# Optimization experiments

Hardware: AMD Instinct MI355X
Metric: run time of the kernel (lower is better)

Reference implementation:

```python
import jax, jax.numpy as jnp
import numpy as np

NF4 = jnp.array([-1.0, -0.6961928009986877, -0.5250730514526367, -0.39491748809814453,
                 -0.28444138169288635, -0.18477343022823334, -0.09105003625154495, 0.0,
                 0.07958029955625534, 0.16093020141124725, 0.24611230194568634,
                 0.33791524171829224, 0.44070982933044434, 0.5626170039176941,
                 0.7229568362236023, 1.0], dtype=jnp.float32)
BLOCK_SIZE = 64
SCALING = 32.0 / 16.0  # alpha / rank


def setup_inputs() -> dict:
    key = jax.random.key(0)
    k = jax.random.split(key, 6)
    B, S, IN, OUT, R = 4, 128, 4096, 11008, 16
    n_blocks = (OUT * IN) // BLOCK_SIZE  # 704512, exact (no padding needed)
    return {
        "x": jax.random.normal(k[0], (B, S, IN), jnp.float32),
        "weight_indices": jax.random.randint(k[1], (OUT, IN), 0, 16, dtype=jnp.int32),
        "weight_scales": jax.random.uniform(k[2], (n_blocks,), jnp.float32),
        "lora_A": jax.random.normal(k[3], (IN, R), jnp.float32),
        "lora_B": jax.random.normal(k[4], (R, OUT), jnp.float32),
        "bias": jax.random.normal(k[5], (OUT,), jnp.float32),
    }


def dequantize_nf4(indices, scales, shape):
    # LUT gather then blockwise absmax scale
    w = NF4[indices.reshape(-1)]                    # [out*in]
    w = w.reshape(-1, BLOCK_SIZE) * scales[:, None]  # [n_blocks, block]
    return w.reshape(shape)                          # [out, in]


def reference(x, weight_indices, weight_scales, lora_A, lora_B, bias):
    W = dequantize_nf4(weight_indices, weight_scales, weight_indices.shape)  # [out, in]
    base = jnp.einsum("bsi,oi->bso", x, W) + bias                            # F.linear
    lora = (x @ lora_A) @ lora_B                                             # low-rank path (dropout p=0 -> identity)
    return base + lora * SCALING
```

## Files before the change

kernel.cpp:

```cpp
#include <hip/hip_runtime.h>
#include <stdint.h>

typedef __bf16 bf16x8 __attribute__((ext_vector_type(8)));
typedef float f32x4 __attribute__((ext_vector_type(4)));
typedef unsigned short ushort_t;

#define N_OUT 11008
#define K_DIM 4096
#define M_DIM 512
#define BM 256
#define BN 64
#define BK 64
#define KHALF 2048
#define NT 32

__constant__ float c_nf4[16] = {
    -1.0f, -0.6961928009986877f, -0.5250730514526367f, -0.39491748809814453f,
    -0.28444138169288635f, -0.18477343022823334f, -0.09105003625154495f, 0.0f,
    0.07958029955625534f, 0.16093020141124725f, 0.24611230194568634f,
    0.33791524171829224f, 0.44070982933044434f, 0.5626170039176941f,
    0.7229568362236023f, 1.0f};

__device__ __forceinline__ uint32_t pkbf(float lo, float hi) {
  uint32_t ul = __builtin_bit_cast(uint32_t, lo);
  uint32_t uh = __builtin_bit_cast(uint32_t, hi);
  return ((ul + 0x8000u) >> 16) | ((uh + 0x8000u) & 0xffff0000u);
}

__device__ __forceinline__ void async16(const void* g, void* l) {
  __builtin_amdgcn_global_load_lds(
      (const __attribute__((address_space(1))) void*)g,
      (__attribute__((address_space(3))) void*)l, 16, 0, 0);
}

__device__ __forceinline__ bf16x8 ldfrag(const ushort_t* p) {
  uint4 r = *reinterpret_cast<const uint4*>(p);
  return __builtin_bit_cast(bf16x8, r);
}

__device__ __forceinline__ uint32_t dq2(int a, int b, float s, const float2* lut) {
  float2 l = lut[a | (b << 4)];
  return pkbf(l.x * s, l.y * s);
}

__global__ void k_prep(const float* __restrict__ x, const float* __restrict__ lA,
                       const float* __restrict__ lB,
                       ushort_t* __restrict__ xbf, ushort_t* __restrict__ xap,
                       ushort_t* __restrict__ btp) {
  const int b = blockIdx.x, t = threadIdx.x;
  if (b < 1024) {
    int oc = b * 256 + t;
    int m = oc >> 9;
    int cr = oc & 511;
    int win = cr >> 3, cp = cr & 7;
    int c = cp ^ (m & 7);
    const float4* s4 = (const float4*)(x + (size_t)m * K_DIM + win * 64 + c * 8);
    float4 v0 = s4[0], v1 = s4[1];
    uint4 o;
    o.x = pkbf(v0.x, v0.y);
    o.y = pkbf(v0.z, v0.w);
    o.z = pkbf(v1.x, v1.y);
    o.w = pkbf(v1.z, v1.w);
    ((uint4*)xbf)[oc] = o;
  } else if (b < 1536) {
    __shared__ float red[256 * 17];
    int m = b - 1024;
    f32x4 ac0 = 0.f, ac1 = 0.f, ac2 = 0.f, ac3 = 0.f;
#pragma unroll
    for (int i = 0; i < 16; ++i) {
      int k = i * 256 + t;
      float xk = x[(size_t)m * K_DIM + k];
      const f32x4* l4 = (const f32x4*)(lA + (size_t)k * 16);
      ac0 += xk * l4[0];
      ac1 += xk * l4[1];
      ac2 += xk * l4[2];
      ac3 += xk * l4[3];
    }
#pragma unroll
    for (int r = 0; r < 4; ++r) {
      red[t * 17 + r] = ac0[r];
      red[t * 17 + 4 + r] = ac1[r];
      red[t * 17 + 8 + r] = ac2[r];
      red[t * 17 + 12 + r] = ac3[r];
    }
    __syncthreads();
#pragma unroll
    for (int s = 128; s >= 16; s >>= 1) {
      if (t < s)
        for (int r = 0; r < 16; ++r) red[t * 17 + r] += red[(t + s) * 17 + r];
      __syncthreads();
    }
    if (t < 32) {
      float v = 0.f;
      if (t < 16) {
        for (int p = 0; p < 16; ++p) v += red[p * 17 + t];
        v *= 2.0f;
      }
      uint32_t u = __builtin_bit_cast(uint32_t, v);
      xap[(size_t)m * 32 + t] = (ushort_t)((u + 0x8000u) >> 16);
    }
  } else {
    int o = (b - 1536) * 256 + t;
    uint32_t p[8];
#pragma unroll
    for (int j = 0; j < 8; ++j)
      p[j] = pkbf(lB[(size_t)(2 * j) * N_OUT + o], lB[(size_t)(2 * j + 1) * N_OUT + o]);
    uint4* dst = reinterpret_cast<uint4*>(btp + (size_t)o * 32);
    dst[0] = make_uint4(p[0], p[1], p[2], p[3]);
    dst[1] = make_uint4(p[4], p[5], p[6], p[7]);
    dst[2] = make_uint4(0u, 0u, 0u, 0u);
    dst[3] = make_uint4(0u, 0u, 0u, 0u);
  }
}

__launch_bounds__(256, 3)
__global__ void k_main(const ushort_t* __restrict__ xbf, const int* __restrict__ wi,
                       const float* __restrict__ sc, const ushort_t* __restrict__ xap,
                       const ushort_t* __restrict__ btp,
                       const float* __restrict__ bias, float* __restrict__ out) {
  __shared__ __align__(16) ushort_t lds_a[BM * BK];
  __shared__ __align__(16) ushort_t lds_b[BN * 72];
  __shared__ float2 lutp[256];

  const int t = threadIdx.x;
  const int lane = t & 63;
  const int w = t >> 6;
  const int o0 = blockIdx.x * BN;
  const int m0 = blockIdx.y * BM;
  const int kh = blockIdx.z;
  const int k0 = kh * KHALF;

  lutp[t] = make_float2(c_nf4[t & 15], c_nf4[t >> 4]);

  const int brow = t >> 2, bq = t & 3;
  const int* gb = wi + (size_t)(o0 + brow) * K_DIM + k0 + bq * 16;
  const float* gs = sc + (size_t)(o0 + brow) * 64 + kh * 32;
  ushort_t* lb = lds_b + brow * 72 + bq * 16;

  const ushort_t* ga =
      xbf + (size_t)(m0 + w * 64 + (lane >> 3)) * K_DIM + k0 + (lane & 7) * 8;
  ushort_t* la_dst = lds_a + w * 4096 + lane * 8;

  const int cl = lane & 15;
  f32x4 acc[4][4];
#pragma unroll
  for (int ni = 0; ni < 4; ++ni) {
    float b0 = (kh == 1) ? bias[o0 + ni * 16 + cl] : 0.f;
#pragma unroll
    for (int mi = 0; mi < 4; ++mi) acc[mi][ni] = (f32x4){b0, b0, b0, b0};
  }

  int4 bi0 = ((const int4*)gb)[0], bi1 = ((const int4*)gb)[1];
  int4 bi2 = ((const int4*)gb)[2], bi3 = ((const int4*)gb)[3];
  float s = gs[0];
  gb += BK;
  uint4 braw;

  const ushort_t* afb = lds_a + (w * 64 + (lane & 15)) * BK;
  const int q = lane >> 4;
  const ushort_t* bfb = lds_b + (lane & 15) * 72 + q * 8;

#pragma unroll 1
  for (int kt = 0; kt < NT; ++kt) {
    __syncthreads();
    uint4 w0, w1;
    w0.x = dq2(bi0.x, bi0.y, s, lutp);
    w0.y = dq2(bi0.z, bi0.w, s, lutp);
    w0.z = dq2(bi1.x, bi1.y, s, lutp);
    w0.w = dq2(bi1.z, bi1.w, s, lutp);
    w1.x = dq2(bi2.x, bi2.y, s, lutp);
    w1.y = dq2(bi2.z, bi2.w, s, lutp);
    w1.z = dq2(bi3.x, bi3.y, s, lutp);
    w1.w = dq2(bi3.z, bi3.w, s, lutp);
    *reinterpret_cast<uint4*>(lb) = w0;
    *reinterpret_cast<uint4*>(lb + 8) = w1;
#pragma unroll
    for (int j = 0; j < 8; ++j)
      async16(ga + (size_t)j * 8 * K_DIM + kt * BK, la_dst + j * 512);
    __syncthreads();
    if (kt + 1 < NT) {
      bi0 = ((const int4*)gb)[0];
      bi1 = ((const int4*)gb)[1];
      bi2 = ((const int4*)gb)[2];
      bi3 = ((const int4*)gb)[3];
      s = gs[kt + 1];
      gb += BK;
    } else if (kh == 1) {
      braw = *reinterpret_cast<const uint4*>(btp + (size_t)(o0 + brow) * 32 + bq * 8);
    }
#pragma unroll
    for (int kc = 0; kc < 2; ++kc) {
      const int cpr = ((kc * 4 + q) ^ (lane & 7)) * 8;
      bf16x8 av[4], bv[4];
#pragma unroll
      for (int mi = 0; mi < 4; ++mi) av[mi] = ldfrag(afb + mi * 16 * BK + cpr);
#pragma unroll
      for (int ni = 0; ni < 4; ++ni) bv[ni] = ldfrag(bfb + ni * 16 * 72 + kc * 32);
#pragma unroll
      for (int mi = 0; mi < 4; ++mi)
#pragma unroll
        for (int ni = 0; ni < 4; ++ni)
          acc[mi][ni] = __builtin_amdgcn_mfma_f32_16x16x32_bf16(av[mi], bv[ni],
                                                                acc[mi][ni], 0, 0, 0);
    }
  }

  if (kh == 1) {
    __syncthreads();
    *reinterpret_cast<uint4*>(lds_b + brow * 72 + bq * 8) = braw;
#pragma unroll
    for (int j = 0; j < 4; ++j)
      async16(xap + (size_t)(m0 + w * 64 + j * 16 + (lane >> 2)) * 32 + (lane & 3) * 8,
              lds_a + w * 2048 + j * 512 + lane * 8);
    __syncthreads();
    bf16x8 av[4], bv[4];
#pragma unroll
    for (int mi = 0; mi < 4; ++mi)
      av[mi] = ldfrag(lds_a + w * 2048 + (mi * 16 + (lane & 15)) * 32 + q * 8);
#pragma unroll
    for (int ni = 0; ni < 4; ++ni)
      bv[ni] = ldfrag(lds_b + (ni * 16 + (lane & 15)) * 72 + q * 8);
#pragma unroll
    for (int mi = 0; mi < 4; ++mi)
#pragma unroll
      for (int ni = 0; ni < 4; ++ni)
        acc[mi][ni] = __builtin_amdgcn_mfma_f32_16x16x32_bf16(av[mi], bv[ni],
                                                              acc[mi][ni], 0, 0, 0);
  }

  const int rg = q * 4;
#pragma unroll
  for (int ni = 0; ni < 4; ++ni) {
    int col = o0 + ni * 16 + cl;
#pragma unroll
    for (int mi = 0; mi < 4; ++mi) {
      int row0 = m0 + w * 64 + mi * 16 + rg;
      float* op = out + (size_t)row0 * N_OUT + col;
#pragma unroll
      for (int i = 0; i < 4; ++i) atomicAdd(op + (size_t)i * N_OUT, acc[mi][ni][i]);
    }
  }
}

extern "C" void kernel_launch(void* const* d_in, const int* in_sizes, int n_in,
                              void* d_out, int out_size, void* d_ws, size_t ws_size,
                              hipStream_t stream) {
  const float* x = (const float*)d_in[0];
  const int* wi = (const int*)d_in[1];
  const float* sc = (const float*)d_in[2];
  const float* lA = (const float*)d_in[3];
  const float* lB = (const float*)d_in[4];
  const float* bias = (const float*)d_in[5];
  float* out = (float*)d_out;

  char* wsb = (char*)d_ws;
  ushort_t* xbf = (ushort_t*)wsb;
  ushort_t* xap = (ushort_t*)(wsb + (4u << 20));
  ushort_t* btp = (ushort_t*)(wsb + (4u << 20) + (32u << 10));

  hipMemsetAsync(out, 0, (size_t)out_size, stream);
  k_prep<<<1579, 256, 0, stream>>>(x, lA, lB, xbf, xap, btp);
  dim3 grid(N_OUT / BN, M_DIM / BM, 2);
  k_main<<<grid, 256, 0, stream>>>(xbf, wi, sc, xap, btp, bias, out);
}
```

Baseline: 347.3 us.

## Pack int32 NF4 indices into nibbles in prep kernel before GEMM

Adds a prep stage that reads the int32 weight indices once and packs them into 4-bit nibbles (two per byte) in workspace. The main GEMM kernel then loads 8 bytes per thread per K-tile instead of 64, and indexes the paired LUT directly by byte. The aim is to cut the weight-index traffic in the main kernel, which is re-read by both M tiles, and to ease register pressure from the large int4 prefetch. The cost is an extra full pass over the 180MB index array plus a packed-buffer write every call.

```diff
diff --git a/kernel.cpp b/kernel.cpp
--- a/kernel.cpp
+++ b/kernel.cpp
@@ -38,18 +38,33 @@
   return __builtin_bit_cast(bf16x8, r);
 }
 
-__device__ __forceinline__ uint32_t dq2(int a, int b, float s, const float2* lut) {
-  float2 l = lut[a | (b << 4)];
+__device__ __forceinline__ uint32_t dqb(uint32_t byte, float s, const float2* lut) {
+  float2 l = lut[byte];
   return pkbf(l.x * s, l.y * s);
 }
 
-__global__ void k_prep(const float* __restrict__ x, const float* __restrict__ lA,
-                       const float* __restrict__ lB,
+__global__ void k_prep(const float* __restrict__ x, const int* __restrict__ wi,
+                       const float* __restrict__ lA, const float* __restrict__ lB,
                        ushort_t* __restrict__ xbf, ushort_t* __restrict__ xap,
-                       ushort_t* __restrict__ btp) {
+                       ushort_t* __restrict__ btp, uint8_t* __restrict__ wpk) {
   const int b = blockIdx.x, t = threadIdx.x;
-  if (b < 1024) {
-    int oc = b * 256 + t;
+  if (b < 11008) {
+    int g = b * 256 + t;
+    int o = g >> 8;
+    int kc = g & 255;
+    const int4* src = (const int4*)(wi + (size_t)o * K_DIM + kc * 16);
+    int4 a0 = src[0], a1 = src[1], a2 = src[2], a3 = src[3];
+    uint32_t lo = (uint32_t)a0.x | ((uint32_t)a0.y << 4) | ((uint32_t)a0.z << 8) |
+                  ((uint32_t)a0.w << 12) | ((uint32_t)a1.x << 16) |
+                  ((uint32_t)a1.y << 20) | ((uint32_t)a1.z << 24) |
+                  ((uint32_t)a1.w << 28);
+    uint32_t hi = (uint32_t)a2.x | ((uint32_t)a2.y << 4) | ((uint32_t)a2.z << 8) |
+                  ((uint32_t)a2.w << 12) | ((uint32_t)a3.x << 16) |
+                  ((uint32_t)a3.y << 20) | ((uint32_t)a3.z << 24) |
+                  ((uint32_t)a3.w << 28);
+    ((uint2*)wpk)[g] = make_uint2(lo, hi);
+  } else if (b < 12032) {
+    int oc = (b - 11008) * 256 + t;
     int m = oc >> 9;
     int cr = oc & 511;
     int win = cr >> 3, cp = cr & 7;
@@ -62,9 +77,9 @@
     o.z = pkbf(v1.x, v1.y);
     o.w = pkbf(v1.z, v1.w);
     ((uint4*)xbf)[oc] = o;
-  } else if (b < 1536) {
+  } else if (b < 12544) {
     __shared__ float red[256 * 17];
-    int m = b - 1024;
+    int m = b - 12032;
     f32x4 ac0 = 0.f, ac1 = 0.f, ac2 = 0.f, ac3 = 0.f;
 #pragma unroll
     for (int i = 0; i < 16; ++i) {
@@ -100,7 +115,7 @@
       xap[(size_t)m * 32 + t] = (ushort_t)((u + 0x8000u) >> 16);
     }
   } else {
-    int o = (b - 1536) * 256 + t;
+    int o = (b - 12544) * 256 + t;
     uint32_t p[8];
 #pragma unroll
     for (int j = 0; j < 8; ++j)
@@ -114,7 +129,7 @@
 }
 
 __launch_bounds__(256, 3)
-__global__ void k_main(const ushort_t* __restrict__ xbf, const int* __restrict__ wi,
+__global__ void k_main(const ushort_t* __restrict__ xbf, const uint8_t* __restrict__ wpk,
                        const float* __restrict__ sc, const ushort_t* __restrict__ xap,
                        const ushort_t* __restrict__ btp,
                        const float* __restrict__ bias, float* __restrict__ out) {
@@ -133,7 +148,8 @@
   lutp[t] = make_float2(c_nf4[t & 15], c_nf4[t >> 4]);
 
   const int brow = t >> 2, bq = t & 3;
-  const int* gb = wi + (size_t)(o0 + brow) * K_DIM + k0 + bq * 16;
+  const uint2* gpb =
+      (const uint2*)(wpk + (size_t)(o0 + brow) * (K_DIM / 2) + (k0 >> 1) + bq * 8);
   const float* gs = sc + (size_t)(o0 + brow) * 64 + kh * 32;
   ushort_t* lb = lds_b + brow * 72 + bq * 16;
 
@@ -150,10 +166,8 @@
     for (int mi = 0; mi < 4; ++mi) acc[mi][ni] = (f32x4){b0, b0, b0, b0};
   }
 
-  int4 bi0 = ((const int4*)gb)[0], bi1 = ((const int4*)gb)[1];
-  int4 bi2 = ((const int4*)gb)[2], bi3 = ((const int4*)gb)[3];
+  uint2 bp = gpb[0];
   float s = gs[0];
-  gb += BK;
   uint4 braw;
 
   const ushort_t* afb = lds_a + (w * 64 + (lane & 15)) * BK;
@@ -163,28 +177,27 @@
 #pragma unroll 1
   for (int kt = 0; kt < NT; ++kt) {
     __syncthreads();
-    uint4 w0, w1;
-    w0.x = dq2(bi0.x, bi0.y, s, lutp);
-    w0.y = dq2(bi0.z, bi0.w, s, lutp);
-    w0.z = dq2(bi1.x, bi1.y, s, lutp);
-    w0.w = dq2(bi1.z, bi1.w, s, lutp);
-    w1.x = dq2(bi2.x, bi2.y, s, lutp);
-    w1.y = dq2(bi2.z, bi2.w, s, lutp);
-    w1.z = dq2(bi3.x, bi3.y, s, lutp);
-    w1.w = dq2(bi3.z, bi3.w, s, lutp);
-    *reinterpret_cast<uint4*>(lb) = w0;
-    *reinterpret_cast<uint4*>(lb + 8) = w1;
+    {
+      uint32_t lo = bp.x, hi = bp.y;
+      uint4 w0, w1;
+      w0.x = dqb(lo & 255u, s, lutp);
+      w0.y = dqb((lo >> 8) & 255u, s, lutp);
+      w0.z = dqb((lo >> 16) & 255u, s, lutp);
+      w0.w = dqb(lo >> 24, s, lutp);
+      w1.x = dqb(hi & 255u, s, lutp);
+      w1.y = dqb((hi >> 8) & 255u, s, lutp);
+      w1.z = dqb((hi >> 16) & 255u, s, lutp);
+      w1.w = dqb(hi >> 24, s, lutp);
+      *reinterpret_cast<uint4*>(lb) = w0;
+      *reinterpret_cast<uint4*>(lb + 8) = w1;
+    }
 #pragma unroll
     for (int j = 0; j < 8; ++j)
       async16(ga + (size_t)j * 8 * K_DIM + kt * BK, la_dst + j * 512);
     __syncthreads();
     if (kt + 1 < NT) {
-      bi0 = ((const int4*)gb)[0];
-      bi1 = ((const int4*)gb)[1];
-      bi2 = ((const int4*)gb)[2];
-      bi3 = ((const int4*)gb)[3];
+      bp = gpb[(kt + 1) * 4];
       s = gs[kt + 1];
-      gb += BK;
     } else if (kh == 1) {
       braw = *reinterpret_cast<const uint4*>(btp + (size_t)(o0 + brow) * 32 + bq * 8);
     }
@@ -257,9 +270,10 @@
   ushort_t* xbf = (ushort_t*)wsb;
   ushort_t* xap = (ushort_t*)(wsb + (4u << 20));
   ushort_t* btp = (ushort_t*)(wsb + (4u << 20) + (32u << 10));
+  uint8_t* wpk = (uint8_t*)(wsb + (5u << 20));
 
   hipMemsetAsync(out, 0, (size_t)out_size, stream);
-  k_prep<<<1579, 256, 0, stream>>>(x, lA, lB, xbf, xap, btp);
+  k_prep<<<12587, 256, 0, stream>>>(x, wi, lA, lB, xbf, xap, btp, wpk);
   dim3 grid(N_OUT / BN, M_DIM / BM, 2);
-  k_main<<<grid, 256, 0, stream>>>(xbf, wi, sc, xap, btp, bias, out);
-}
+  k_main<<<grid, 256, 0, stream>>>(xbf, wpk, sc, xap, btp, bias, out);
+}
```

New measurement: 374.7 us. +7.9%, slower.

## Double-buffer weight LDS tile, remap blocks for XCD locality, batch prep work

Applied to the files above, without the earlier changes.

The dequantized weight tile in LDS now uses two alternating buffers, so the barrier at the top of each K iteration can go; one barrier per iteration remains. The 3D grid becomes a 1D grid of 688 blocks, remapped so that blocks sharing the same weight rows (both M halves and both K halves) land on the same XCD, which should improve L2 reuse of the int32 weight indices. The prep kernel has each thread convert four x chunks instead of one, cutting its block count. The cost is extra LDS for the second weight buffer, which could affect the occupancy of three blocks per CU. Dropping the barrier relies on each wave's A tile region being private to that wave.

```diff
diff --git a/kernel.cpp b/kernel.cpp
--- a/kernel.cpp
+++ b/kernel.cpp
@@ -13,6 +13,7 @@
 #define BK 64
 #define KHALF 2048
 #define NT 32
+#define BSTRIDE (BN * 72)
 
 __constant__ float c_nf4[16] = {
     -1.0f, -0.6961928009986877f, -0.5250730514526367f, -0.39491748809814453f,
@@ -48,23 +49,27 @@
                        ushort_t* __restrict__ xbf, ushort_t* __restrict__ xap,
                        ushort_t* __restrict__ btp) {
   const int b = blockIdx.x, t = threadIdx.x;
-  if (b < 1024) {
-    int oc = b * 256 + t;
-    int m = oc >> 9;
-    int cr = oc & 511;
-    int win = cr >> 3, cp = cr & 7;
-    int c = cp ^ (m & 7);
-    const float4* s4 = (const float4*)(x + (size_t)m * K_DIM + win * 64 + c * 8);
-    float4 v0 = s4[0], v1 = s4[1];
-    uint4 o;
-    o.x = pkbf(v0.x, v0.y);
-    o.y = pkbf(v0.z, v0.w);
-    o.z = pkbf(v1.x, v1.y);
-    o.w = pkbf(v1.z, v1.w);
-    ((uint4*)xbf)[oc] = o;
-  } else if (b < 1536) {
+  if (b < 256) {
+    int base = b * 1024 + t;
+#pragma unroll
+    for (int i = 0; i < 4; ++i) {
+      int oc = base + i * 256;
+      int m = oc >> 9;
+      int cr = oc & 511;
+      int win = cr >> 3, cp = cr & 7;
+      int c = cp ^ (m & 7);
+      const float4* s4 = (const float4*)(x + (size_t)m * K_DIM + win * 64 + c * 8);
+      float4 v0 = s4[0], v1 = s4[1];
+      uint4 o;
+      o.x = pkbf(v0.x, v0.y);
+      o.y = pkbf(v0.z, v0.w);
+      o.z = pkbf(v1.x, v1.y);
+      o.w = pkbf(v1.z, v1.w);
+      ((uint4*)xbf)[oc] = o;
+    }
+  } else if (b < 768) {
     __shared__ float red[256 * 17];
-    int m = b - 1024;
+    int m = b - 256;
     f32x4 ac0 = 0.f, ac1 = 0.f, ac2 = 0.f, ac3 = 0.f;
 #pragma unroll
     for (int i = 0; i < 16; ++i) {
@@ -100,7 +105,7 @@
       xap[(size_t)m * 32 + t] = (ushort_t)((u + 0x8000u) >> 16);
     }
   } else {
-    int o = (b - 1536) * 256 + t;
+    int o = (b - 768) * 256 + t;
     uint32_t p[8];
 #pragma unroll
     for (int j = 0; j < 8; ++j)
@@ -119,15 +124,18 @@
                        const ushort_t* __restrict__ btp,
                        const float* __restrict__ bias, float* __restrict__ out) {
   __shared__ __align__(16) ushort_t lds_a[BM * BK];
-  __shared__ __align__(16) ushort_t lds_b[BN * 72];
+  __shared__ __align__(16) ushort_t lds_b[2][BSTRIDE];
   __shared__ float2 lutp[256];
 
   const int t = threadIdx.x;
   const int lane = t & 63;
   const int w = t >> 6;
-  const int o0 = blockIdx.x * BN;
-  const int m0 = blockIdx.y * BM;
-  const int kh = blockIdx.z;
+
+  const int n = blockIdx.x;
+  const int wg = (n & 7) * 86 + (n >> 3);
+  const int o0 = (wg >> 2) * BN;
+  const int kh = (wg >> 1) & 1;
+  const int m0 = (wg & 1) * BM;
   const int k0 = kh * KHALF;
 
   lutp[t] = make_float2(c_nf4[t & 15], c_nf4[t >> 4]);
@@ -135,7 +143,7 @@
   const int brow = t >> 2, bq = t & 3;
   const int* gb = wi + (size_t)(o0 + brow) * K_DIM + k0 + bq * 16;
   const float* gs = sc + (size_t)(o0 + brow) * 64 + kh * 32;
-  ushort_t* lb = lds_b + brow * 72 + bq * 16;
+  ushort_t* lb = &lds_b[0][brow * 72 + bq * 16];
 
   const ushort_t* ga =
       xbf + (size_t)(m0 + w * 64 + (lane >> 3)) * K_DIM + k0 + (lane & 7) * 8;
@@ -158,22 +166,26 @@
 
   const ushort_t* afb = lds_a + (w * 64 + (lane & 15)) * BK;
   const int q = lane >> 4;
-  const ushort_t* bfb = lds_b + (lane & 15) * 72 + q * 8;
+  const ushort_t* bfb = &lds_b[0][(lane & 15) * 72 + q * 8];
+
+  __syncthreads();
 
 #pragma unroll 1
   for (int kt = 0; kt < NT; ++kt) {
-    __syncthreads();
-    uint4 w0, w1;
-    w0.x = dq2(bi0.x, bi0.y, s, lutp);
-    w0.y = dq2(bi0.z, bi0.w, s, lutp);
-    w0.z = dq2(bi1.x, bi1.y, s, lutp);
-    w0.w = dq2(bi1.z, bi1.w, s, lutp);
-    w1.x = dq2(bi2.x, bi2.y, s, lutp);
-    w1.y = dq2(bi2.z, bi2.w, s, lutp);
-    w1.z = dq2(bi3.x, bi3.y, s, lutp);
-    w1.w = dq2(bi3.z, bi3.w, s, lutp);
-    *reinterpret_cast<uint4*>(lb) = w0;
-    *reinterpret_cast<uint4*>(lb + 8) = w1;
+    {
+      uint4 w0, w1;
+      w0.x = dq2(bi0.x, bi0.y, s, lutp);
+      w0.y = dq2(bi0.z, bi0.w, s, lutp);
+      w0.z = dq2(bi1.x, bi1.y, s, lutp);
+      w0.w = dq2(bi1.z, bi1.w, s, lutp);
+      w1.x = dq2(bi2.x, bi2.y, s, lutp);
+      w1.y = dq2(bi2.z, bi2.w, s, lutp);
+      w1.z = dq2(bi3.x, bi3.y, s, lutp);
+      w1.w = dq2(bi3.z, bi3.w, s, lutp);
+      ushort_t* lbk = lb + (kt & 1) * BSTRIDE;
+      *reinterpret_cast<uint4*>(lbk) = w0;
+      *reinterpret_cast<uint4*>(lbk + 8) = w1;
+    }
 #pragma unroll
     for (int j = 0; j < 8; ++j)
       async16(ga + (size_t)j * 8 * K_DIM + kt * BK, la_dst + j * 512);
@@ -188,6 +200,7 @@
     } else if (kh == 1) {
       braw = *reinterpret_cast<const uint4*>(btp + (size_t)(o0 + brow) * 32 + bq * 8);
     }
+    const ushort_t* bfbk = bfb + (kt & 1) * BSTRIDE;
 #pragma unroll
     for (int kc = 0; kc < 2; ++kc) {
       const int cpr = ((kc * 4 + q) ^ (lane & 7)) * 8;
@@ -195,7 +208,7 @@
 #pragma unroll
       for (int mi = 0; mi < 4; ++mi) av[mi] = ldfrag(afb + mi * 16 * BK + cpr);
 #pragma unroll
-      for (int ni = 0; ni < 4; ++ni) bv[ni] = ldfrag(bfb + ni * 16 * 72 + kc * 32);
+      for (int ni = 0; ni < 4; ++ni) bv[ni] = ldfrag(bfbk + ni * 16 * 72 + kc * 32);
 #pragma unroll
       for (int mi = 0; mi < 4; ++mi)
 #pragma unroll
@@ -207,7 +220,7 @@
 
   if (kh == 1) {
     __syncthreads();
-    *reinterpret_cast<uint4*>(lds_b + brow * 72 + bq * 8) = braw;
+    *reinterpret_cast<uint4*>(&lds_b[0][brow * 72 + bq * 8]) = braw;
 #pragma unroll
     for (int j = 0; j < 4; ++j)
       async16(xap + (size_t)(m0 + w * 64 + j * 16 + (lane >> 2)) * 32 + (lane & 3) * 8,
@@ -219,7 +232,7 @@
       av[mi] = ldfrag(lds_a + w * 2048 + (mi * 16 + (lane & 15)) * 32 + q * 8);
 #pragma unroll
     for (int ni = 0; ni < 4; ++ni)
-      bv[ni] = ldfrag(lds_b + (ni * 16 + (lane & 15)) * 72 + q * 8);
+      bv[ni] = ldfrag(&lds_b[0][(ni * 16 + (lane & 15)) * 72 + q * 8]);
 #pragma unroll
     for (int mi = 0; mi < 4; ++mi)
 #pragma unroll
@@ -259,7 +272,6 @@
   ushort_t* btp = (ushort_t*)(wsb + (4u << 20) + (32u << 10));
 
   hipMemsetAsync(out, 0, (size_t)out_size, stream);
-  k_prep<<<1579, 256, 0, stream>>>(x, lA, lB, xbf, xap, btp);
-  dim3 grid(N_OUT / BN, M_DIM / BM, 2);
-  k_main<<<grid, 256, 0, stream>>>(xbf, wi, sc, xap, btp, bias, out);
-}
+  k_prep<<<811, 256, 0, stream>>>(x, lA, lB, xbf, xap, btp);
+  k_main<<<688, 256, 0, stream>>>(xbf, wi, sc, xap, btp, bias, out);
+}
```

Measured after the change: 341.4 us. No clear change (-1.7%).
